# Kernel optimization log

Hardware: AMD Instinct MI355X
Metric: run time of the kernel (lower is better)

Reference implementation:

```python
import jax, jax.numpy as jnp
import numpy as np

N = 50000      # num nodes
E = 800000     # num edges
IN = 128       # in_channels
OUT = 128      # out_channels
H = 8          # num_heads
HD = OUT // H  # out_channels_conv (per-head dim)
EDIM = 16      # edge_dim
HID = 512      # hidden_dim of dst MLP


def layer_norm(x, w, b, eps=1e-5):
    m = jnp.mean(x, axis=-1, keepdims=True)
    v = jnp.var(x, axis=-1, keepdims=True)
    return (x - m) * jax.lax.rsqrt(v + eps) * w + b


def setup_inputs() -> dict:
    key = jax.random.key(0)
    ks = jax.random.split(key, 16)
    lin = lambda k, i, o: jax.random.normal(k, (i, o), jnp.float32) / np.sqrt(i)
    return {
        "x": jax.random.normal(ks[0], (N, IN), jnp.float32),
        "edge_attr": jax.random.normal(ks[1], (E, EDIM), jnp.float32),
        "edge_index": jax.random.randint(ks[2], (2, E), 0, N),
        "Wq": lin(ks[3], IN, OUT), "bq": jnp.zeros((OUT,), jnp.float32),
        "Wk": lin(ks[4], IN, OUT), "bk": jnp.zeros((OUT,), jnp.float32),
        "Wv": lin(ks[5], IN, OUT), "bv": jnp.zeros((OUT,), jnp.float32),
        "Ws": lin(ks[6], IN, OUT), "bs": jnp.zeros((OUT,), jnp.float32),
        "We": lin(ks[7], EDIM, OUT), "be": jnp.zeros((OUT,), jnp.float32),
        "Wp": lin(ks[8], OUT, OUT), "bp": jnp.zeros((OUT,), jnp.float32),
        "ln_a_w": jnp.ones((IN,), jnp.float32), "ln_a_b": jnp.zeros((IN,), jnp.float32),
        "ln_m_w": jnp.ones((OUT,), jnp.float32), "ln_m_b": jnp.zeros((OUT,), jnp.float32),
        "W1": lin(ks[9], OUT, HID), "b1": jnp.zeros((HID,), jnp.float32),
        "W2": lin(ks[10], HID, OUT), "b2": jnp.zeros((OUT,), jnp.float32),
    }


def reference(x, edge_attr, edge_index, Wq, bq, Wk, bk, Wv, bv, Ws, bs, We, be,
              Wp, bp, ln_a_w, ln_a_b, ln_m_w, ln_m_b, W1, b1, W2, b2):
    src, dst = edge_index[0], edge_index[1]

    x_skip = x
    xn = layer_norm(x, ln_a_w, ln_a_b)           # pre-attention LN
    x_r = xn @ Ws + bs                           # lin_self

    q = (xn @ Wq + bq).reshape(N, H, HD)
    k = (xn @ Wk + bk).reshape(N, H, HD)
    v = (xn @ Wv + bv).reshape(N, H, HD)
    e = (edge_attr @ We + be).reshape(E, H, HD)

    # edge-indexed attention: score(edge) = <q[dst], k[src]+e> / sqrt(HD)
    kj = k[src] + e                                              # [E,H,HD]
    scores = jnp.einsum('ehd,ehd->eh', q[dst], kj) / np.sqrt(HD)  # [E,H]

    # segment softmax over incoming edges of each dst node
    smax = jax.ops.segment_max(scores, dst, num_segments=N)     # [N,H]
    smax = jnp.where(jnp.isfinite(smax), smax, 0.0)             # guard empty segments
    ex = jnp.exp(scores - smax[dst])                            # [E,H]
    denom = jax.ops.segment_sum(ex, dst, num_segments=N)        # [N,H]
    alpha = ex / jnp.maximum(denom[dst], 1e-16)                 # [E,H]

    msg = (v[src] + e) * alpha[..., None]                       # [E,H,HD]
    out = jax.ops.segment_sum(msg, dst, num_segments=N).reshape(N, OUT)

    out = (out + x_r) @ Wp + bp                                 # projection
    out = out + x_skip                                          # residual

    # dst-node MLP with pre-LN and residual
    h = layer_norm(out, ln_m_w, ln_m_b)
    nodes_new = jax.nn.gelu(h @ W1 + b1) @ W2 + b2 + out
    return nodes_new, edge_attr
```

## Files before the change

kernel.cpp:

```cpp
#include <hip/hip_runtime.h>
#include <math.h>

#define N_NODES 50000
#define N_EDGES 800000

typedef __attribute__((ext_vector_type(8))) short bf16x8;
typedef __attribute__((ext_vector_type(4))) float f32x4;

__device__ __forceinline__ short f2bf(float f){
  unsigned u = __float_as_uint(f);
  unsigned r = (u + 0x7FFFu + ((u >> 16) & 1u)) >> 16;
  return (short)r;
}

__device__ __forceinline__ float gelu_f(float x){
  float z = 0.7978845608028654f*(x + 0.044715f*x*x*x);
  float e = __expf(2.0f*z);
  return 0.5f*x*(2.0f - 2.0f/(e + 1.0f));
}

__global__ __launch_bounds__(256) void k_tconv(const float* __restrict__ W, short* __restrict__ Wt,
                                               int K, int Nn){
  int i = blockIdx.x*256 + threadIdx.x;
  if (i < K*Nn){
    int n = i / K, k = i - n*K;
    Wt[(size_t)n*K + k] = f2bf(W[(size_t)k*Nn + n]);
  }
}

struct TC6 { const float* src[6]; short* dst[6]; };
__global__ __launch_bounds__(256) void k_tconv6(TC6 t){
  int b = blockIdx.y;
  const float* W = t.src[b];
  short* Wt = t.dst[b];
  int i = blockIdx.x*256 + threadIdx.x;
  int n = i >> 7, k = i & 127;
  Wt[n*128 + k] = f2bf(W[k*128 + n]);
}

__global__ __launch_bounds__(256) void k_wqm(const float* __restrict__ Wq, const float* __restrict__ We,
                                             const float* __restrict__ bq,
                                             float* __restrict__ Wqm, float* __restrict__ bqm){
  int i = blockIdx.x*256 + threadIdx.x;
  if (i < 16384){
    int k = i >> 7, j = i & 127;
    int h = j >> 4, c = j & 15;
    float s = 0.f;
    #pragma unroll
    for (int dd = 0; dd < 16; ++dd)
      s += Wq[k*128 + h*16 + dd] * We[c*128 + h*16 + dd];
    Wqm[i] = s;
    if (k == 0){
      float t = 0.f;
      #pragma unroll
      for (int dd = 0; dd < 16; ++dd)
        t += bq[h*16 + dd] * We[c*128 + h*16 + dd];
      bqm[j] = t;
    }
  }
}

__global__ __launch_bounds__(256) void k_deg(const int* __restrict__ dst, int* __restrict__ deg){
  int i = blockIdx.x*256 + threadIdx.x;
  if (i < N_EDGES) atomicAdd(&deg[dst[i]], 1);
}

__global__ __launch_bounds__(256) void k_bsum(const int* __restrict__ deg,
                                              int* __restrict__ bsum, int* __restrict__ hist){
  __shared__ int lhist[64];
  __shared__ int wred[4];
  int tid = threadIdx.x;
  int i = blockIdx.x*256 + tid;
  if (tid < 64) lhist[tid] = 0;
  __syncthreads();
  int v = (i < N_NODES) ? deg[i] : 0;
  if (i < N_NODES) atomicAdd(&lhist[v > 63 ? 63 : v], 1);
  int s = v;
  #pragma unroll
  for (int sh = 32; sh >= 1; sh >>= 1) s += __shfl_xor(s, sh, 64);
  if ((tid & 63) == 0) wred[tid >> 6] = s;
  __syncthreads();
  if (tid == 0) bsum[blockIdx.x] = wred[0] + wred[1] + wred[2] + wred[3];
  if (tid < 64){ int c = lhist[tid]; if (c) atomicAdd(&hist[tid], c); }
}

__global__ __launch_bounds__(256) void k_bscan(const int* __restrict__ bsum, int* __restrict__ bbase,
                                               const int* __restrict__ hist, int* __restrict__ histcur){
  __shared__ int wsum[4];
  int tid = threadIdx.x;
  int v = (tid < 196) ? bsum[tid] : 0;
  int incl = v;
  #pragma unroll
  for (int s = 1; s < 64; s <<= 1){
    int t = __shfl_up(incl, s, 64);
    if ((tid & 63) >= s) incl += t;
  }
  if ((tid & 63) == 63) wsum[tid >> 6] = incl;
  __syncthreads();
  if (tid == 0){ int c = 0; for (int j = 0; j < 4; ++j){ int t = wsum[j]; wsum[j] = c; c += t; } }
  __syncthreads();
  if (tid < 196) bbase[tid] = wsum[tid >> 6] + (incl - v);
  if (tid < 64){
    int h = hist[tid];
    int inc = h;
    #pragma unroll
    for (int s = 1; s < 64; s <<= 1){
      int t = __shfl_up(inc, s, 64);
      if (tid >= s) inc += t;
    }
    int total = __shfl(inc, 63, 64);
    histcur[tid] = total - inc;
  }
}

__global__ __launch_bounds__(256) void k_apply(const int* __restrict__ deg, const int* __restrict__ bbase,
                                               int* __restrict__ off, int* __restrict__ cursor){
  __shared__ int wsum[4];
  int tid = threadIdx.x;
  int i = blockIdx.x*256 + tid;
  int v = (i < N_NODES) ? deg[i] : 0;
  int incl = v;
  #pragma unroll
  for (int s = 1; s < 64; s <<= 1){
    int t = __shfl_up(incl, s, 64);
    if ((tid & 63) >= s) incl += t;
  }
  if ((tid & 63) == 63) wsum[tid >> 6] = incl;
  __syncthreads();
  if (tid == 0){ int c = 0; for (int j = 0; j < 4; ++j){ int t = wsum[j]; wsum[j] = c; c += t; } }
  __syncthreads();
  int excl = bbase[blockIdx.x] + wsum[tid >> 6] + (incl - v);
  if (i < N_NODES){
    off[i] = excl; cursor[i] = excl;
    if (i == N_NODES-1) off[N_NODES] = excl + v;
  }
}

__global__ __launch_bounds__(256) void k_scatter(const int* __restrict__ dst, const int* __restrict__ src,
                                                 int* __restrict__ cursor, int2* __restrict__ ebuf){
  int i = blockIdx.x*256 + threadIdx.x;
  if (i < N_EDGES){
    int d = dst[i];
    int pos = atomicAdd(&cursor[d], 1);
    ebuf[pos] = make_int2(src[i], i);
  }
}

__global__ __launch_bounds__(256) void k_perm(const int* __restrict__ deg, const int* __restrict__ off,
                                              int* __restrict__ histcur,
                                              int* __restrict__ perm, int2* __restrict__ rng){
  __shared__ int lhist[64];
  __shared__ int lbase[64];
  int tid = threadIdx.x;
  int i = blockIdx.x*256 + tid;
  if (tid < 64) lhist[tid] = 0;
  __syncthreads();
  int d = 0, b = 0, loc = 0;
  bool ok = i < N_NODES;
  if (ok){
    d = deg[i];
    b = d > 63 ? 63 : d;
    loc = atomicAdd(&lhist[b], 1);
  }
  __syncthreads();
  if (tid < 64){
    int c = lhist[tid];
    lbase[tid] = c ? atomicAdd(&histcur[tid], c) : 0;
  }
  __syncthreads();
  if (ok){
    int pos = lbase[b] + loc;
    perm[pos] = i;
    int o = off[i];
    rng[pos] = make_int2(o, o + d);
  }
}

__global__ __launch_bounds__(256) void k_nodeproj(
  const float* __restrict__ x, const float* __restrict__ lnw, const float* __restrict__ lnb,
  const short* __restrict__ Wtq, const short* __restrict__ Wtqm,
  const short* __restrict__ Wtk, const short* __restrict__ Wtv, const short* __restrict__ Wts,
  const float* __restrict__ bq, const float* __restrict__ bqm,
  const float* __restrict__ bk, const float* __restrict__ bv, const float* __restrict__ bs,
  ushort* __restrict__ qb, ushort* __restrict__ qweb,
  ushort* __restrict__ kb, ushort* __restrict__ vb, float* __restrict__ xr)
{
  __shared__ short A[64][136];
  int tid = threadIdx.x;
  int rbase = blockIdx.x * 64;

  {
    int r = tid >> 2, j = tid & 3;
    int row = rbase + r;
    bool ok = row < N_NODES;
    const float* xp = x + (size_t)row*128 + j*32;
    float vals[32];
    #pragma unroll
    for (int i = 0; i < 8; ++i){
      float4 t = ok ? *(const float4*)(xp + i*4) : make_float4(0,0,0,0);
      vals[i*4+0]=t.x; vals[i*4+1]=t.y; vals[i*4+2]=t.z; vals[i*4+3]=t.w;
    }
    float s = 0.f, s2 = 0.f;
    #pragma unroll
    for (int i = 0; i < 32; ++i){ s += vals[i]; s2 += vals[i]*vals[i]; }
    s  += __shfl_xor(s, 1, 64);  s  += __shfl_xor(s, 2, 64);
    s2 += __shfl_xor(s2, 1, 64); s2 += __shfl_xor(s2, 2, 64);
    float mean = s * 0.0078125f;
    float var  = s2 * 0.0078125f - mean*mean;
    float rstd = rsqrtf(var + 1e-5f);
    #pragma unroll
    for (int i = 0; i < 32; ++i){
      int col = j*32 + i;
      float xn = (vals[i]-mean)*rstd*lnw[col] + lnb[col];
      A[r][col] = f2bf(xn);
    }
  }
  __syncthreads();

  int lane = tid & 63, wave = tid >> 6;
  int row16 = lane & 15, kg = lane >> 4;
  int cb = wave * 32;

  auto gemm = [&](const short* __restrict__ B, const float* __restrict__ bias,
                  float* __restrict__ Of, ushort* __restrict__ Ob){
    f32x4 acc[4][2] = {};
    #pragma unroll
    for (int kk = 0; kk < 128; kk += 32){
      int k0 = kk + kg*8;
      bf16x8 a0 = *(const bf16x8*)&A[ 0 + row16][k0];
      bf16x8 a1 = *(const bf16x8*)&A[16 + row16][k0];
      bf16x8 a2 = *(const bf16x8*)&A[32 + row16][k0];
      bf16x8 a3 = *(const bf16x8*)&A[48 + row16][k0];
      bf16x8 b0 = *(const bf16x8*)&B[(size_t)(cb +      row16)*128 + k0];
      bf16x8 b1 = *(const bf16x8*)&B[(size_t)(cb + 16 + row16)*128 + k0];
      acc[0][0] = __builtin_amdgcn_mfma_f32_16x16x32_bf16(a0, b0, acc[0][0], 0,0,0);
      acc[1][0] = __builtin_amdgcn_mfma_f32_16x16x32_bf16(a1, b0, acc[1][0], 0,0,0);
      acc[2][0] = __builtin_amdgcn_mfma_f32_16x16x32_bf16(a2, b0, acc[2][0], 0,0,0);
      acc[3][0] = __builtin_amdgcn_mfma_f32_16x16x32_bf16(a3, b0, acc[3][0], 0,0,0);
      acc[0][1] = __builtin_amdgcn_mfma_f32_16x16x32_bf16(a0, b1, acc[0][1], 0,0,0);
      acc[1][1] = __builtin_amdgcn_mfma_f32_16x16x32_bf16(a1, b1, acc[1][1], 0,0,0);
      acc[2][1] = __builtin_amdgcn_mfma_f32_16x16x32_bf16(a2, b1, acc[2][1], 0,0,0);
      acc[3][1] = __builtin_amdgcn_mfma_f32_16x16x32_bf16(a3, b1, acc[3][1], 0,0,0);
    }
    float bv0 = bias[cb + row16], bv1 = bias[cb + 16 + row16];
    #pragma unroll
    for (int rt = 0; rt < 4; ++rt){
      #pragma unroll
      for (int i = 0; i < 4; ++i){
        int row = rbase + rt*16 + kg*4 + i;
        if (row < N_NODES){
          float v0 = acc[rt][0][i] + bv0;
          float v1 = acc[rt][1][i] + bv1;
          if (Of){
            Of[(size_t)row*128 + cb      + row16] = v0;
            Of[(size_t)row*128 + cb + 16 + row16] = v1;
          } else {
            Ob[(size_t)row*128 + cb      + row16] = (ushort)f2bf(v0);
            Ob[(size_t)row*128 + cb + 16 + row16] = (ushort)f2bf(v1);
          }
        }
      }
    }
  };
  gemm(Wtq,  bq,  nullptr, qb);
  gemm(Wtqm, bqm, nullptr, qweb);
  gemm(Wtk,  bk,  nullptr, kb);
  gemm(Wtv,  bv,  nullptr, vb);
  gemm(Wts,  bs,  xr,  nullptr);
}

__global__ __launch_bounds__(256) void k_agg(
  const ushort* __restrict__ qb, const ushort* __restrict__ qweb,
  const ushort* __restrict__ kbf, const ushort* __restrict__ vbf,
  const float* __restrict__ edge_attr, const float* __restrict__ We, const float* __restrict__ be,
  const int2* __restrict__ ebuf, const int* __restrict__ perm, const int2* __restrict__ rng,
  float* __restrict__ xr)
{
  int tid = threadIdx.x;
  int gid = blockIdx.x*8 + (tid >> 5);
  int node = perm[gid];
  int2 r = rng[gid];
  int beg = r.x, end = r.y;
  int l = tid & 31;
  int d0 = l*4;
  int h  = l >> 2;
  int c0 = (l & 3)*4;

  uint2 qw = *(const uint2*)&qb[(size_t)node*128 + d0];
  float4 qv = make_float4(__uint_as_float(qw.x<<16), __uint_as_float(qw.x&0xffff0000u),
                          __uint_as_float(qw.y<<16), __uint_as_float(qw.y&0xffff0000u));
  uint2 qew = *(const uint2*)&qweb[(size_t)node*128 + h*16 + c0];
  float4 qe = make_float4(__uint_as_float(qew.x<<16), __uint_as_float(qew.x&0xffff0000u),
                          __uint_as_float(qew.y<<16), __uint_as_float(qew.y&0xffff0000u));
  float m = -INFINITY, den = 0.f;
  float4 va = make_float4(0,0,0,0);
  float4 S  = make_float4(0,0,0,0);

  int p = beg;
  for (; p + 4 <= end; p += 4){
    int2 pr0 = ebuf[p+0];
    int2 pr1 = ebuf[p+1];
    int2 pr2 = ebuf[p+2];
    int2 pr3 = ebuf[p+3];
    uint2 kw0 = *(const uint2*)&kbf[(size_t)pr0.x*128 + d0];
    uint2 kw1 = *(const uint2*)&kbf[(size_t)pr1.x*128 + d0];
    uint2 kw2 = *(const uint2*)&kbf[(size_t)pr2.x*128 + d0];
    uint2 kw3 = *(const uint2*)&kbf[(size_t)pr3.x*128 + d0];
    uint2 vw0 = *(const uint2*)&vbf[(size_t)pr0.x*128 + d0];
    uint2 vw1 = *(const uint2*)&vbf[(size_t)pr1.x*128 + d0];
    uint2 vw2 = *(const uint2*)&vbf[(size_t)pr2.x*128 + d0];
    uint2 vw3 = *(const uint2*)&vbf[(size_t)pr3.x*128 + d0];
    float4 e0 = *(const float4*)&edge_attr[(size_t)pr0.y*16 + c0];
    float4 e1 = *(const float4*)&edge_attr[(size_t)pr1.y*16 + c0];
    float4 e2 = *(const float4*)&edge_attr[(size_t)pr2.y*16 + c0];
    float4 e3 = *(const float4*)&edge_attr[(size_t)pr3.y*16 + c0];

    float p0 = qv.x*__uint_as_float(kw0.x<<16) + qv.y*__uint_as_float(kw0.x&0xffff0000u)
             + qv.z*__uint_as_float(kw0.y<<16) + qv.w*__uint_as_float(kw0.y&0xffff0000u)
             + qe.x*e0.x + qe.y*e0.y + qe.z*e0.z + qe.w*e0.w;
    float p1 = qv.x*__uint_as_float(kw1.x<<16) + qv.y*__uint_as_float(kw1.x&0xffff0000u)
             + qv.z*__uint_as_float(kw1.y<<16) + qv.w*__uint_as_float(kw1.y&0xffff0000u)
             + qe.x*e1.x + qe.y*e1.y + qe.z*e1.z + qe.w*e1.w;
    float p2 = qv.x*__uint_as_float(kw2.x<<16) + qv.y*__uint_as_float(kw2.x&0xffff0000u)
             + qv.z*__uint_as_float(kw2.y<<16) + qv.w*__uint_as_float(kw2.y&0xffff0000u)
             + qe.x*e2.x + qe.y*e2.y + qe.z*e2.z + qe.w*e2.w;
    float p3 = qv.x*__uint_as_float(kw3.x<<16) + qv.y*__uint_as_float(kw3.x&0xffff0000u)
             + qv.z*__uint_as_float(kw3.y<<16) + qv.w*__uint_as_float(kw3.y&0xffff0000u)
             + qe.x*e3.x + qe.y*e3.y + qe.z*e3.z + qe.w*e3.w;
    p0 += __shfl_xor(p0,1,64); p0 += __shfl_xor(p0,2,64);
    p1 += __shfl_xor(p1,1,64); p1 += __shfl_xor(p1,2,64);
    p2 += __shfl_xor(p2,1,64); p2 += __shfl_xor(p2,2,64);
    p3 += __shfl_xor(p3,1,64); p3 += __shfl_xor(p3,2,64);
    float sc0 = p0*0.25f, sc1 = p1*0.25f, sc2 = p2*0.25f, sc3 = p3*0.25f;
    float mn = fmaxf(fmaxf(m, fmaxf(sc0,sc1)), fmaxf(sc2,sc3));
    float corr = __expf(m - mn);
    float w0 = __expf(sc0 - mn), w1 = __expf(sc1 - mn);
    float w2 = __expf(sc2 - mn), w3 = __expf(sc3 - mn);
    den = den*corr + ((w0+w1)+(w2+w3));
    va.x = va.x*corr + (w0*__uint_as_float(vw0.x<<16)        + w1*__uint_as_float(vw1.x<<16))
                     + (w2*__uint_as_float(vw2.x<<16)        + w3*__uint_as_float(vw3.x<<16));
    va.y = va.y*corr + (w0*__uint_as_float(vw0.x&0xffff0000u)+ w1*__uint_as_float(vw1.x&0xffff0000u))
                     + (w2*__uint_as_float(vw2.x&0xffff0000u)+ w3*__uint_as_float(vw3.x&0xffff0000u));
    va.z = va.z*corr + (w0*__uint_as_float(vw0.y<<16)        + w1*__uint_as_float(vw1.y<<16))
                     + (w2*__uint_as_float(vw2.y<<16)        + w3*__uint_as_float(vw3.y<<16));
    va.w = va.w*corr + (w0*__uint_as_float(vw0.y&0xffff0000u)+ w1*__uint_as_float(vw1.y&0xffff0000u))
                     + (w2*__uint_as_float(vw2.y&0xffff0000u)+ w3*__uint_as_float(vw3.y&0xffff0000u));
    S.x = S.x*corr + (w0*e0.x + w1*e1.x) + (w2*e2.x + w3*e3.x);
    S.y = S.y*corr + (w0*e0.y + w1*e1.y) + (w2*e2.y + w3*e3.y);
    S.z = S.z*corr + (w0*e0.z + w1*e1.z) + (w2*e2.z + w3*e3.z);
    S.w = S.w*corr + (w0*e0.w + w1*e1.w) + (w2*e2.w + w3*e3.w);
    m = mn;
  }
  for (; p < end; ++p){
    int2 pr = ebuf[p];
    uint2 kw = *(const uint2*)&kbf[(size_t)pr.x*128 + d0];
    uint2 vw = *(const uint2*)&vbf[(size_t)pr.x*128 + d0];
    float4 ev = *(const float4*)&edge_attr[(size_t)pr.y*16 + c0];
    float pp = qv.x*__uint_as_float(kw.x<<16) + qv.y*__uint_as_float(kw.x&0xffff0000u)
             + qv.z*__uint_as_float(kw.y<<16) + qv.w*__uint_as_float(kw.y&0xffff0000u)
             + qe.x*ev.x + qe.y*ev.y + qe.z*ev.z + qe.w*ev.w;
    pp += __shfl_xor(pp,1,64); pp += __shfl_xor(pp,2,64);
    float sc = pp*0.25f;
    float mn = fmaxf(m, sc);
    float corr = __expf(m - mn);
    float pe = __expf(sc - mn);
    den = den*corr + pe;
    va.x = va.x*corr + pe*__uint_as_float(vw.x<<16);
    va.y = va.y*corr + pe*__uint_as_float(vw.x&0xffff0000u);
    va.z = va.z*corr + pe*__uint_as_float(vw.y<<16);
    va.w = va.w*corr + pe*__uint_as_float(vw.y&0xffff0000u);
    S.x = S.x*corr + pe*ev.x;
    S.y = S.y*corr + pe*ev.y;
    S.z = S.z*corr + pe*ev.z;
    S.w = S.w*corr + pe*ev.w;
    m = mn;
  }

  if (end > beg){
    float inv = 1.0f/den;
    float4 acc = va;
    int gb = (tid & 63) & 60;
    #pragma unroll
    for (int g = 0; g < 4; ++g){
      float s0 = __shfl(S.x, gb+g, 64);
      float s1 = __shfl(S.y, gb+g, 64);
      float s2 = __shfl(S.z, gb+g, 64);
      float s3 = __shfl(S.w, gb+g, 64);
      float4 w0 = *(const float4*)&We[(g*4+0)*128 + d0];
      float4 w1 = *(const float4*)&We[(g*4+1)*128 + d0];
      float4 w2 = *(const float4*)&We[(g*4+2)*128 + d0];
      float4 w3 = *(const float4*)&We[(g*4+3)*128 + d0];
      acc.x += s0*w0.x + s1*w1.x + s2*w2.x + s3*w3.x;
      acc.y += s0*w0.y + s1*w1.y + s2*w2.y + s3*w3.y;
      acc.z += s0*w0.z + s1*w1.z + s2*w2.z + s3*w3.z;
      acc.w += s0*w0.w + s1*w1.w + s2*w2.w + s3*w3.w;
    }
    float4 bev = *(const float4*)&be[d0];
    float4 xv = *(const float4*)&xr[(size_t)node*128 + d0];
    xv.x += acc.x*inv + bev.x;
    xv.y += acc.y*inv + bev.y;
    xv.z += acc.z*inv + bev.z;
    xv.w += acc.w*inv + bev.w;
    *(float4*)&xr[(size_t)node*128 + d0] = xv;
  }
}

__global__ __launch_bounds__(256) void k_post(
  const float* __restrict__ aggout, const float* __restrict__ x,
  const short* __restrict__ Wtp, const float* __restrict__ bp,
  const float* __restrict__ lnw, const float* __restrict__ lnb,
  float* __restrict__ res, short* __restrict__ A2)
{
  __shared__ short A[64][136];
  __shared__ float rf[64][132];
  int tid = threadIdx.x;
  int rbase = blockIdx.x * 64;

  {
    int r = tid >> 2, j = tid & 3;
    int row = rbase + r;
    const float* p = aggout + (size_t)row*128 + j*32;
    #pragma unroll
    for (int i = 0; i < 8; ++i){
      float4 t = *(const float4*)(p + i*4);
      int c = j*32 + i*4;
      A[r][c+0] = f2bf(t.x); A[r][c+1] = f2bf(t.y);
      A[r][c+2] = f2bf(t.z); A[r][c+3] = f2bf(t.w);
    }
  }
  __syncthreads();

  int lane = tid & 63, wave = tid >> 6;
  int row16 = lane & 15, kg = lane >> 4;
  int cb = wave * 32;

  f32x4 acc[4][2] = {};
  #pragma unroll
  for (int kk = 0; kk < 128; kk += 32){
    int k0 = kk + kg*8;
    bf16x8 a0 = *(const bf16x8*)&A[ 0 + row16][k0];
    bf16x8 a1 = *(const bf16x8*)&A[16 + row16][k0];
    bf16x8 a2 = *(const bf16x8*)&A[32 + row16][k0];
    bf16x8 a3 = *(const bf16x8*)&A[48 + row16][k0];
    bf16x8 b0 = *(const bf16x8*)&Wtp[(size_t)(cb +      row16)*128 + k0];
    bf16x8 b1 = *(const bf16x8*)&Wtp[(size_t)(cb + 16 + row16)*128 + k0];
    acc[0][0] = __builtin_amdgcn_mfma_f32_16x16x32_bf16(a0, b0, acc[0][0], 0,0,0);
    acc[1][0] = __builtin_amdgcn_mfma_f32_16x16x32_bf16(a1, b0, acc[1][0], 0,0,0);
    acc[2][0] = __builtin_amdgcn_mfma_f32_16x16x32_bf16(a2, b0, acc[2][0], 0,0,0);
    acc[3][0] = __builtin_amdgcn_mfma_f32_16x16x32_bf16(a3, b0, acc[3][0], 0,0,0);
    acc[0][1] = __builtin_amdgcn_mfma_f32_16x16x32_bf16(a0, b1, acc[0][1], 0,0,0);
    acc[1][1] = __builtin_amdgcn_mfma_f32_16x16x32_bf16(a1, b1, acc[1][1], 0,0,0);
    acc[2][1] = __builtin_amdgcn_mfma_f32_16x16x32_bf16(a2, b1, acc[2][1], 0,0,0);
    acc[3][1] = __builtin_amdgcn_mfma_f32_16x16x32_bf16(a3, b1, acc[3][1], 0,0,0);
  }
  float bv0 = bp[cb + row16], bv1 = bp[cb + 16 + row16];
  #pragma unroll
  for (int rt = 0; rt < 4; ++rt){
    #pragma unroll
    for (int i = 0; i < 4; ++i){
      int rl = rt*16 + kg*4 + i;
      int row = rbase + rl;
      float v0 = acc[rt][0][i] + bv0;
      float v1 = acc[rt][1][i] + bv1;
      if (row < N_NODES){
        v0 += x[(size_t)row*128 + cb      + row16];
        v1 += x[(size_t)row*128 + cb + 16 + row16];
        res[(size_t)row*128 + cb      + row16] = v0;
        res[(size_t)row*128 + cb + 16 + row16] = v1;
      }
      rf[rl][cb      + row16] = v0;
      rf[rl][cb + 16 + row16] = v1;
    }
  }
  __syncthreads();

  {
    int r = tid >> 2, j = tid & 3;
    int row = rbase + r;
    float vals[32];
    #pragma unroll
    for (int i = 0; i < 8; ++i){
      float4 t = *(const float4*)&rf[r][j*32 + i*4];
      vals[i*4+0]=t.x; vals[i*4+1]=t.y; vals[i*4+2]=t.z; vals[i*4+3]=t.w;
    }
    float s = 0.f, s2 = 0.f;
    #pragma unroll
    for (int i = 0; i < 32; ++i){ s += vals[i]; s2 += vals[i]*vals[i]; }
    s  += __shfl_xor(s, 1, 64);  s  += __shfl_xor(s, 2, 64);
    s2 += __shfl_xor(s2, 1, 64); s2 += __shfl_xor(s2, 2, 64);
    float mean = s * 0.0078125f;
    float var  = s2 * 0.0078125f - mean*mean;
    float rstd = rsqrtf(var + 1e-5f);
    #pragma unroll
    for (int i = 0; i < 32; ++i){
      int col = j*32 + i;
      float xn = (vals[i]-mean)*rstd*lnw[col] + lnb[col];
      A2[(size_t)row*128 + col] = f2bf(xn);
    }
  }
}

__global__ __launch_bounds__(256) void k_mlp1(
  const short* __restrict__ A2, const short* __restrict__ W1t, const float* __restrict__ b1,
  short* __restrict__ hid)
{
  __shared__ short A[64][136];
  int tid = threadIdx.x;
  int rbase = blockIdx.x * 64;
  int ch = blockIdx.y;
  for (int idx = tid; idx < 1024; idx += 256){
    int r = idx >> 4, g = idx & 15;
    *(uint4*)&A[r][g*8] = *(const uint4*)&A2[((size_t)(rbase + r))*128 + g*8];
  }
  __syncthreads();

  int lane = tid & 63, wave = tid >> 6;
  int row16 = lane & 15, kg = lane >> 4;
  int cb = ch*256 + wave*64;

  f32x4 acc[4][4] = {};
  #pragma unroll
  for (int kk = 0; kk < 128; kk += 32){
    int k0 = kk + kg*8;
    bf16x8 a[4], b[4];
    #pragma unroll
    for (int rt = 0; rt < 4; ++rt) a[rt] = *(const bf16x8*)&A[rt*16 + row16][k0];
    #pragma unroll
    for (int ct = 0; ct < 4; ++ct) b[ct] = *(const bf16x8*)&W1t[(size_t)(cb + ct*16 + row16)*128 + k0];
    #pragma unroll
    for (int rt = 0; rt < 4; ++rt)
      #pragma unroll
      for (int ct = 0; ct < 4; ++ct)
        acc[rt][ct] = __builtin_amdgcn_mfma_f32_16x16x32_bf16(a[rt], b[ct], acc[rt][ct], 0,0,0);
  }
  float bv[4];
  #pragma unroll
  for (int ct = 0; ct < 4; ++ct) bv[ct] = b1[cb + ct*16 + row16];
  #pragma unroll
  for (int rt = 0; rt < 4; ++rt){
    #pragma unroll
    for (int ct = 0; ct < 4; ++ct){
      #pragma unroll
      for (int i = 0; i < 4; ++i){
        int row = rbase + rt*16 + kg*4 + i;
        hid[(size_t)row*512 + cb + ct*16 + row16] = f2bf(gelu_f(acc[rt][ct][i] + bv[ct]));
      }
    }
  }
}

__global__ __launch_bounds__(256) void k_mlp2(
  const short* __restrict__ hid, const short* __restrict__ W2t, const float* __restrict__ b2,
  const float* __restrict__ res, float* __restrict__ out)
{
  __shared__ short A[64][136];
  int tid = threadIdx.x;
  int rbase = blockIdx.x * 64;
  int lane = tid & 63, wave = tid >> 6;
  int row16 = lane & 15, kg = lane >> 4;
  int cb = wave * 32;

  f32x4 acc[4][2] = {};
  for (int kc = 0; kc < 4; ++kc){
    __syncthreads();
    for (int idx = tid; idx < 1024; idx += 256){
      int r = idx >> 4, g = idx & 15;
      *(uint4*)&A[r][g*8] = *(const uint4*)&hid[((size_t)(rbase + r))*512 + kc*128 + g*8];
    }
    __syncthreads();
    #pragma unroll
    for (int kk = 0; kk < 128; kk += 32){
      int k0 = kk + kg*8;
      bf16x8 a0 = *(const bf16x8*)&A[ 0 + row16][k0];
      bf16x8 a1 = *(const bf16x8*)&A[16 + row16][k0];
      bf16x8 a2 = *(const bf16x8*)&A[32 + row16][k0];
      bf16x8 a3 = *(const bf16x8*)&A[48 + row16][k0];
      bf16x8 b0 = *(const bf16x8*)&W2t[(size_t)(cb +      row16)*512 + kc*128 + k0];
      bf16x8 b1 = *(const bf16x8*)&W2t[(size_t)(cb + 16 + row16)*512 + kc*128 + k0];
      acc[0][0] = __builtin_amdgcn_mfma_f32_16x16x32_bf16(a0, b0, acc[0][0], 0,0,0);
      acc[1][0] = __builtin_amdgcn_mfma_f32_16x16x32_bf16(a1, b0, acc[1][0], 0,0,0);
      acc[2][0] = __builtin_amdgcn_mfma_f32_16x16x32_bf16(a2, b0, acc[2][0], 0,0,0);
      acc[3][0] = __builtin_amdgcn_mfma_f32_16x16x32_bf16(a3, b0, acc[3][0], 0,0,0);
      acc[0][1] = __builtin_amdgcn_mfma_f32_16x16x32_bf16(a0, b1, acc[0][1], 0,0,0);
      acc[1][1] = __builtin_amdgcn_mfma_f32_16x16x32_bf16(a1, b1, acc[1][1], 0,0,0);
      acc[2][1] = __builtin_amdgcn_mfma_f32_16x16x32_bf16(a2, b1, acc[2][1], 0,0,0);
      acc[3][1] = __builtin_amdgcn_mfma_f32_16x16x32_bf16(a3, b1, acc[3][1], 0,0,0);
    }
  }
  float bv0 = b2[cb + row16], bv1 = b2[cb + 16 + row16];
  #pragma unroll
  for (int rt = 0; rt < 4; ++rt){
    #pragma unroll
    for (int i = 0; i < 4; ++i){
      int row = rbase + rt*16 + kg*4 + i;
      if (row < N_NODES){
        out[(size_t)row*128 + cb      + row16] = acc[rt][0][i] + bv0 + res[(size_t)row*128 + cb      + row16];
        out[(size_t)row*128 + cb + 16 + row16] = acc[rt][1][i] + bv1 + res[(size_t)row*128 + cb + 16 + row16];
      }
    }
  }
}

extern "C" void kernel_launch(void* const* d_in, const int* in_sizes, int n_in,
                              void* d_out, int out_size, void* d_ws, size_t ws_size,
                              hipStream_t stream)
{
  const float* x        = (const float*)d_in[0];
  const float* edge_attr= (const float*)d_in[1];
  const int*   edge_index=(const int*)d_in[2];
  const float* Wq = (const float*)d_in[3];  const float* bq = (const float*)d_in[4];
  const float* Wk = (const float*)d_in[5];  const float* bk = (const float*)d_in[6];
  const float* Wv = (const float*)d_in[7];  const float* bv = (const float*)d_in[8];
  const float* Wss= (const float*)d_in[9];  const float* bss= (const float*)d_in[10];
  const float* We = (const float*)d_in[11]; const float* be = (const float*)d_in[12];
  const float* Wp = (const float*)d_in[13]; const float* bp = (const float*)d_in[14];
  const float* lnaw=(const float*)d_in[15]; const float* lnab=(const float*)d_in[16];
  const float* lnmw=(const float*)d_in[17]; const float* lnmb=(const float*)d_in[18];
  const float* W1 = (const float*)d_in[19]; const float* b1 = (const float*)d_in[20];
  const float* W2 = (const float*)d_in[21]; const float* b2 = (const float*)d_in[22];

  float* ws = (float*)d_ws;
  const size_t NP128 = 6406144;
  const size_t NPH   = 3203072;
  ushort* qb   = (ushort*)ws;
  ushort* qweb = (ushort*)(ws + NPH);
  ushort* kbf  = (ushort*)(ws + 2*NPH);
  ushort* vbf  = (ushort*)(ws + 3*NPH);
  float*  xr   = ws + 4*NPH;
  float*  res  = ws + 4*NPH + NP128;
  short* wts   = (short*)(ws + 25624576);
  short* Wtq   = wts;
  short* Wtk   = wts + 16384;
  short* Wtv   = wts + 32768;
  short* Wts_  = wts + 49152;
  short* Wtp   = wts + 65536;
  short* Wtqm  = wts + 81920;
  short* W1t   = wts + 98304;
  short* W2t   = wts + 163840;
  float* Wqm_f = ws + 25624576 + 114688;
  float* bqm   = Wqm_f + 16384;
  int*   iw    = (int*)(bqm + 128);
  int* deg     = iw;
  int* hist    = iw + 50000;
  int* histcur = iw + 50064;
  int* bsum    = iw + 50128;
  int* bbase   = iw + 50324;
  int* off     = iw + 50520;
  int* cursor  = iw + 100521;
  int* perm    = iw + 150521;
  int2* rng    = (int2*)(iw + 200522);
  int2* ebuf   = (int2*)(iw + 300522);

  short* A2   = (short*)qb;
  short* hid  = (short*)qweb;

  const int* srcIdx = edge_index;
  const int* dstIdx = edge_index + N_EDGES;

  k_wqm<<<64, 256, 0, stream>>>(Wq, We, bq, Wqm_f, bqm);
  TC6 tc;
  tc.src[0]=Wq; tc.src[1]=Wk; tc.src[2]=Wv; tc.src[3]=Wss; tc.src[4]=Wp; tc.src[5]=Wqm_f;
  tc.dst[0]=Wtq; tc.dst[1]=Wtk; tc.dst[2]=Wtv; tc.dst[3]=Wts_; tc.dst[4]=Wtp; tc.dst[5]=Wtqm;
  k_tconv6<<<dim3(64,6), 256, 0, stream>>>(tc);
  k_tconv<<<256, 256, 0, stream>>>(W1, W1t, 128, 512);
  k_tconv<<<256, 256, 0, stream>>>(W2, W2t, 512, 128);

  hipMemsetAsync(deg, 0, 50064*sizeof(int), stream);
  k_deg<<<(N_EDGES+255)/256, 256, 0, stream>>>(dstIdx, deg);
  k_bsum<<<196, 256, 0, stream>>>(deg, bsum, hist);
  k_bscan<<<1, 256, 0, stream>>>(bsum, bbase, hist, histcur);
  k_apply<<<196, 256, 0, stream>>>(deg, bbase, off, cursor);
  k_scatter<<<(N_EDGES+255)/256, 256, 0, stream>>>(dstIdx, srcIdx, cursor, ebuf);
  k_perm<<<(N_NODES+255)/256, 256, 0, stream>>>(deg, off, histcur, perm, rng);

  k_nodeproj<<<782, 256, 0, stream>>>(x, lnaw, lnab, Wtq, Wtqm, Wtk, Wtv, Wts_,
                                      bq, bqm, bk, bv, bss, qb, qweb, kbf, vbf, xr);
  k_agg<<<N_NODES/8, 256, 0, stream>>>(qb, qweb, kbf, vbf, edge_attr, We, be,
                                       ebuf, perm, rng, xr);
  k_post<<<782, 256, 0, stream>>>(xr, x, Wtp, bp, lnmw, lnmb, res, A2);
  k_mlp1<<<dim3(782,2), 256, 0, stream>>>(A2, W1t, b1, hid);
  k_mlp2<<<782, 256, 0, stream>>>(hid, W2t, b2, res, (float*)d_out);

  hipMemcpyAsync((float*)d_out + (size_t)N_NODES*128, edge_attr,
                 (size_t)N_EDGES*16*sizeof(float), hipMemcpyDeviceToDevice, stream);
}
```

Before: 369.9 us.

## Pre-sort edge attributes to bf16 in CSR order and unroll aggregation by eight

The scatter kernel now writes each edge's attributes, converted to bf16 and placed in dst-sorted order, into a scratch buffer that aliases the residual workspace. The aggregation kernel then reads these contiguously instead of gathering fp32 rows by original edge id, and reads only the source index from a smaller int array. The aggregation main loop is also unrolled to 8 edges, with a 4-edge step after it. This aims to cut gather traffic and random access in the aggregation kernel, at the cost of extra write traffic in scatter and some loss of precision from rounding edge features to bf16.

```diff
diff --git a/kernel.cpp b/kernel.cpp
--- a/kernel.cpp
+++ b/kernel.cpp
@@ -12,12 +12,18 @@
   unsigned r = (u + 0x7FFFu + ((u >> 16) & 1u)) >> 16;
   return (short)r;
 }
+__device__ __forceinline__ unsigned pkbf(float lo, float hi){
+  return (unsigned)(unsigned short)f2bf(lo) | ((unsigned)(unsigned short)f2bf(hi) << 16);
+}
 
 __device__ __forceinline__ float gelu_f(float x){
   float z = 0.7978845608028654f*(x + 0.044715f*x*x*x);
   float e = __expf(2.0f*z);
   return 0.5f*x*(2.0f - 2.0f/(e + 1.0f));
 }
+
+#define BF_LO(u) __uint_as_float((u)<<16)
+#define BF_HI(u) __uint_as_float((u)&0xffff0000u)
 
 __global__ __launch_bounds__(256) void k_tconv(const float* __restrict__ W, short* __restrict__ Wt,
                                                int K, int Nn){
@@ -137,12 +143,22 @@
 }
 
 __global__ __launch_bounds__(256) void k_scatter(const int* __restrict__ dst, const int* __restrict__ src,
-                                                 int* __restrict__ cursor, int2* __restrict__ ebuf){
+                                                 const float* __restrict__ edge_attr,
+                                                 int* __restrict__ cursor,
+                                                 int* __restrict__ esrc, ushort* __restrict__ eab){
   int i = blockIdx.x*256 + threadIdx.x;
   if (i < N_EDGES){
     int d = dst[i];
     int pos = atomicAdd(&cursor[d], 1);
-    ebuf[pos] = make_int2(src[i], i);
+    esrc[pos] = src[i];
+    const float* ea = edge_attr + (size_t)i*16;
+    float4 a = *(const float4*)(ea+0), b = *(const float4*)(ea+4),
+           c = *(const float4*)(ea+8), e = *(const float4*)(ea+12);
+    uint4 o0, o1;
+    o0.x = pkbf(a.x,a.y); o0.y = pkbf(a.z,a.w); o0.z = pkbf(b.x,b.y); o0.w = pkbf(b.z,b.w);
+    o1.x = pkbf(c.x,c.y); o1.y = pkbf(c.z,c.w); o1.z = pkbf(e.x,e.y); o1.w = pkbf(e.z,e.w);
+    *(uint4*)&eab[(size_t)pos*16]     = o0;
+    *(uint4*)&eab[(size_t)pos*16 + 8] = o1;
   }
 }
 
@@ -272,8 +288,8 @@
 __global__ __launch_bounds__(256) void k_agg(
   const ushort* __restrict__ qb, const ushort* __restrict__ qweb,
   const ushort* __restrict__ kbf, const ushort* __restrict__ vbf,
-  const float* __restrict__ edge_attr, const float* __restrict__ We, const float* __restrict__ be,
-  const int2* __restrict__ ebuf, const int* __restrict__ perm, const int2* __restrict__ rng,
+  const ushort* __restrict__ eab, const float* __restrict__ We, const float* __restrict__ be,
+  const int* __restrict__ esrc, const int* __restrict__ perm, const int2* __restrict__ rng,
   float* __restrict__ xr)
 {
   int tid = threadIdx.x;
@@ -287,92 +303,85 @@
   int c0 = (l & 3)*4;
 
   uint2 qw = *(const uint2*)&qb[(size_t)node*128 + d0];
-  float4 qv = make_float4(__uint_as_float(qw.x<<16), __uint_as_float(qw.x&0xffff0000u),
-                          __uint_as_float(qw.y<<16), __uint_as_float(qw.y&0xffff0000u));
+  float4 qv = make_float4(BF_LO(qw.x), BF_HI(qw.x), BF_LO(qw.y), BF_HI(qw.y));
   uint2 qew = *(const uint2*)&qweb[(size_t)node*128 + h*16 + c0];
-  float4 qe = make_float4(__uint_as_float(qew.x<<16), __uint_as_float(qew.x&0xffff0000u),
-                          __uint_as_float(qew.y<<16), __uint_as_float(qew.y&0xffff0000u));
+  float4 qe = make_float4(BF_LO(qew.x), BF_HI(qew.x), BF_LO(qew.y), BF_HI(qew.y));
   float m = -INFINITY, den = 0.f;
   float4 va = make_float4(0,0,0,0);
   float4 S  = make_float4(0,0,0,0);
 
   int p = beg;
-  for (; p + 4 <= end; p += 4){
-    int2 pr0 = ebuf[p+0];
-    int2 pr1 = ebuf[p+1];
-    int2 pr2 = ebuf[p+2];
-    int2 pr3 = ebuf[p+3];
-    uint2 kw0 = *(const uint2*)&kbf[(size_t)pr0.x*128 + d0];
-    uint2 kw1 = *(const uint2*)&kbf[(size_t)pr1.x*128 + d0];
-    uint2 kw2 = *(const uint2*)&kbf[(size_t)pr2.x*128 + d0];
-    uint2 kw3 = *(const uint2*)&kbf[(size_t)pr3.x*128 + d0];
-    uint2 vw0 = *(const uint2*)&vbf[(size_t)pr0.x*128 + d0];
-    uint2 vw1 = *(const uint2*)&vbf[(size_t)pr1.x*128 + d0];
-    uint2 vw2 = *(const uint2*)&vbf[(size_t)pr2.x*128 + d0];
-    uint2 vw3 = *(const uint2*)&vbf[(size_t)pr3.x*128 + d0];
-    float4 e0 = *(const float4*)&edge_attr[(size_t)pr0.y*16 + c0];
-    float4 e1 = *(const float4*)&edge_attr[(size_t)pr1.y*16 + c0];
-    float4 e2 = *(const float4*)&edge_attr[(size_t)pr2.y*16 + c0];
-    float4 e3 = *(const float4*)&edge_attr[(size_t)pr3.y*16 + c0];
-
-    float p0 = qv.x*__uint_as_float(kw0.x<<16) + qv.y*__uint_as_float(kw0.x&0xffff0000u)
-             + qv.z*__uint_as_float(kw0.y<<16) + qv.w*__uint_as_float(kw0.y&0xffff0000u)
-             + qe.x*e0.x + qe.y*e0.y + qe.z*e0.z + qe.w*e0.w;
-    float p1 = qv.x*__uint_as_float(kw1.x<<16) + qv.y*__uint_as_float(kw1.x&0xffff0000u)
-             + qv.z*__uint_as_float(kw1.y<<16) + qv.w*__uint_as_float(kw1.y&0xffff0000u)
-             + qe.x*e1.x + qe.y*e1.y + qe.z*e1.z + qe.w*e1.w;
-    float p2 = qv.x*__uint_as_float(kw2.x<<16) + qv.y*__uint_as_float(kw2.x&0xffff0000u)
-             + qv.z*__uint_as_float(kw2.y<<16) + qv.w*__uint_as_float(kw2.y&0xffff0000u)
-             + qe.x*e2.x + qe.y*e2.y + qe.z*e2.z + qe.w*e2.w;
-    float p3 = qv.x*__uint_as_float(kw3.x<<16) + qv.y*__uint_as_float(kw3.x&0xffff0000u)
-             + qv.z*__uint_as_float(kw3.y<<16) + qv.w*__uint_as_float(kw3.y&0xffff0000u)
-             + qe.x*e3.x + qe.y*e3.y + qe.z*e3.z + qe.w*e3.w;
-    p0 += __shfl_xor(p0,1,64); p0 += __shfl_xor(p0,2,64);
-    p1 += __shfl_xor(p1,1,64); p1 += __shfl_xor(p1,2,64);
-    p2 += __shfl_xor(p2,1,64); p2 += __shfl_xor(p2,2,64);
-    p3 += __shfl_xor(p3,1,64); p3 += __shfl_xor(p3,2,64);
-    float sc0 = p0*0.25f, sc1 = p1*0.25f, sc2 = p2*0.25f, sc3 = p3*0.25f;
-    float mn = fmaxf(fmaxf(m, fmaxf(sc0,sc1)), fmaxf(sc2,sc3));
-    float corr = __expf(m - mn);
-    float w0 = __expf(sc0 - mn), w1 = __expf(sc1 - mn);
-    float w2 = __expf(sc2 - mn), w3 = __expf(sc3 - mn);
-    den = den*corr + ((w0+w1)+(w2+w3));
-    va.x = va.x*corr + (w0*__uint_as_float(vw0.x<<16)        + w1*__uint_as_float(vw1.x<<16))
-                     + (w2*__uint_as_float(vw2.x<<16)        + w3*__uint_as_float(vw3.x<<16));
-    va.y = va.y*corr + (w0*__uint_as_float(vw0.x&0xffff0000u)+ w1*__uint_as_float(vw1.x&0xffff0000u))
-                     + (w2*__uint_as_float(vw2.x&0xffff0000u)+ w3*__uint_as_float(vw3.x&0xffff0000u));
-    va.z = va.z*corr + (w0*__uint_as_float(vw0.y<<16)        + w1*__uint_as_float(vw1.y<<16))
-                     + (w2*__uint_as_float(vw2.y<<16)        + w3*__uint_as_float(vw3.y<<16));
-    va.w = va.w*corr + (w0*__uint_as_float(vw0.y&0xffff0000u)+ w1*__uint_as_float(vw1.y&0xffff0000u))
-                     + (w2*__uint_as_float(vw2.y&0xffff0000u)+ w3*__uint_as_float(vw3.y&0xffff0000u));
-    S.x = S.x*corr + (w0*e0.x + w1*e1.x) + (w2*e2.x + w3*e3.x);
-    S.y = S.y*corr + (w0*e0.y + w1*e1.y) + (w2*e2.y + w3*e3.y);
-    S.z = S.z*corr + (w0*e0.z + w1*e1.z) + (w2*e2.z + w3*e3.z);
-    S.w = S.w*corr + (w0*e0.w + w1*e1.w) + (w2*e2.w + w3*e3.w);
-    m = mn;
-  }
+
+#define AGG_STEP(J)                                                            \
+  {                                                                            \
+    int sidx[J];                                                               \
+    _Pragma("unroll")                                                          \
+    for (int j = 0; j < J; ++j) sidx[j] = esrc[p+j];                           \
+    uint2 kw[J], vw[J], ew[J];                                                 \
+    _Pragma("unroll")                                                          \
+    for (int j = 0; j < J; ++j){                                               \
+      kw[j] = *(const uint2*)&kbf[(size_t)sidx[j]*128 + d0];                   \
+      vw[j] = *(const uint2*)&vbf[(size_t)sidx[j]*128 + d0];                   \
+      ew[j] = *(const uint2*)&eab[(size_t)(p+j)*16 + c0];                      \
+    }                                                                          \
+    float sc[J];                                                               \
+    _Pragma("unroll")                                                          \
+    for (int j = 0; j < J; ++j){                                               \
+      float pp = qv.x*BF_LO(kw[j].x) + qv.y*BF_HI(kw[j].x)                     \
+               + qv.z*BF_LO(kw[j].y) + qv.w*BF_HI(kw[j].y)                     \
+               + qe.x*BF_LO(ew[j].x) + qe.y*BF_HI(ew[j].x)                     \
+               + qe.z*BF_LO(ew[j].y) + qe.w*BF_HI(ew[j].y);                    \
+      pp += __shfl_xor(pp,1,64); pp += __shfl_xor(pp,2,64);                    \
+      sc[j] = pp*0.25f;                                                        \
+    }                                                                          \
+    float mn = m;                                                              \
+    _Pragma("unroll")                                                          \
+    for (int j = 0; j < J; ++j) mn = fmaxf(mn, sc[j]);                         \
+    float corr = __expf(m - mn);                                               \
+    float w[J]; float ds = 0.f;                                                \
+    _Pragma("unroll")                                                          \
+    for (int j = 0; j < J; ++j){ w[j] = __expf(sc[j]-mn); ds += w[j]; }        \
+    den = den*corr + ds;                                                       \
+    float ax=0.f, ay=0.f, az=0.f, aw2=0.f, sx=0.f, sy=0.f, sz=0.f, sw=0.f;     \
+    _Pragma("unroll")                                                          \
+    for (int j = 0; j < J; ++j){                                               \
+      ax += w[j]*BF_LO(vw[j].x); ay += w[j]*BF_HI(vw[j].x);                    \
+      az += w[j]*BF_LO(vw[j].y); aw2+= w[j]*BF_HI(vw[j].y);                    \
+      sx += w[j]*BF_LO(ew[j].x); sy += w[j]*BF_HI(ew[j].x);                    \
+      sz += w[j]*BF_LO(ew[j].y); sw += w[j]*BF_HI(ew[j].y);                    \
+    }                                                                          \
+    va.x = va.x*corr + ax; va.y = va.y*corr + ay;                              \
+    va.z = va.z*corr + az; va.w = va.w*corr + aw2;                             \
+    S.x  = S.x *corr + sx; S.y  = S.y *corr + sy;                              \
+    S.z  = S.z *corr + sz; S.w  = S.w *corr + sw;                              \
+    m = mn;                                                                    \
+  }
+
+  for (; p + 8 <= end; p += 8) AGG_STEP(8)
+  for (; p + 4 <= end; p += 4) AGG_STEP(4)
   for (; p < end; ++p){
-    int2 pr = ebuf[p];
-    uint2 kw = *(const uint2*)&kbf[(size_t)pr.x*128 + d0];
-    uint2 vw = *(const uint2*)&vbf[(size_t)pr.x*128 + d0];
-    float4 ev = *(const float4*)&edge_attr[(size_t)pr.y*16 + c0];
-    float pp = qv.x*__uint_as_float(kw.x<<16) + qv.y*__uint_as_float(kw.x&0xffff0000u)
-             + qv.z*__uint_as_float(kw.y<<16) + qv.w*__uint_as_float(kw.y&0xffff0000u)
-             + qe.x*ev.x + qe.y*ev.y + qe.z*ev.z + qe.w*ev.w;
+    int s = esrc[p];
+    uint2 kw = *(const uint2*)&kbf[(size_t)s*128 + d0];
+    uint2 vw = *(const uint2*)&vbf[(size_t)s*128 + d0];
+    uint2 ew = *(const uint2*)&eab[(size_t)p*16 + c0];
+    float pp = qv.x*BF_LO(kw.x) + qv.y*BF_HI(kw.x)
+             + qv.z*BF_LO(kw.y) + qv.w*BF_HI(kw.y)
+             + qe.x*BF_LO(ew.x) + qe.y*BF_HI(ew.x)
+             + qe.z*BF_LO(ew.y) + qe.w*BF_HI(ew.y);
     pp += __shfl_xor(pp,1,64); pp += __shfl_xor(pp,2,64);
     float sc = pp*0.25f;
     float mn = fmaxf(m, sc);
     float corr = __expf(m - mn);
     float pe = __expf(sc - mn);
     den = den*corr + pe;
-    va.x = va.x*corr + pe*__uint_as_float(vw.x<<16);
-    va.y = va.y*corr + pe*__uint_as_float(vw.x&0xffff0000u);
-    va.z = va.z*corr + pe*__uint_as_float(vw.y<<16);
-    va.w = va.w*corr + pe*__uint_as_float(vw.y&0xffff0000u);
-    S.x = S.x*corr + pe*ev.x;
-    S.y = S.y*corr + pe*ev.y;
-    S.z = S.z*corr + pe*ev.z;
-    S.w = S.w*corr + pe*ev.w;
+    va.x = va.x*corr + pe*BF_LO(vw.x);
+    va.y = va.y*corr + pe*BF_HI(vw.x);
+    va.z = va.z*corr + pe*BF_LO(vw.y);
+    va.w = va.w*corr + pe*BF_HI(vw.y);
+    S.x = S.x*corr + pe*BF_LO(ew.x);
+    S.y = S.y*corr + pe*BF_HI(ew.x);
+    S.z = S.z*corr + pe*BF_LO(ew.y);
+    S.w = S.w*corr + pe*BF_HI(ew.y);
     m = mn;
   }
 
@@ -628,6 +637,7 @@
   ushort* vbf  = (ushort*)(ws + 3*NPH);
   float*  xr   = ws + 4*NPH;
   float*  res  = ws + 4*NPH + NP128;
+  ushort* eab  = (ushort*)res;
   short* wts   = (short*)(ws + 25624576);
   short* Wtq   = wts;
   short* Wtk   = wts + 16384;
@@ -649,7 +659,7 @@
   int* cursor  = iw + 100521;
   int* perm    = iw + 150521;
   int2* rng    = (int2*)(iw + 200522);
-  int2* ebuf   = (int2*)(iw + 300522);
+  int* esrc    = iw + 300522;
 
   short* A2   = (short*)qb;
   short* hid  = (short*)qweb;
@@ -670,13 +680,13 @@
   k_bsum<<<196, 256, 0, stream>>>(deg, bsum, hist);
   k_bscan<<<1, 256, 0, stream>>>(bsum, bbase, hist, histcur);
   k_apply<<<196, 256, 0, stream>>>(deg, bbase, off, cursor);
-  k_scatter<<<(N_EDGES+255)/256, 256, 0, stream>>>(dstIdx, srcIdx, cursor, ebuf);
+  k_scatter<<<(N_EDGES+255)/256, 256, 0, stream>>>(dstIdx, srcIdx, edge_attr, cursor, esrc, eab);
   k_perm<<<(N_NODES+255)/256, 256, 0, stream>>>(deg, off, histcur, perm, rng);
 
   k_nodeproj<<<782, 256, 0, stream>>>(x, lnaw, lnab, Wtq, Wtqm, Wtk, Wtv, Wts_,
                                       bq, bqm, bk, bv, bss, qb, qweb, kbf, vbf, xr);
-  k_agg<<<N_NODES/8, 256, 0, stream>>>(qb, qweb, kbf, vbf, edge_attr, We, be,
-                                       ebuf, perm, rng, xr);
+  k_agg<<<N_NODES/8, 256, 0, stream>>>(qb, qweb, kbf, vbf, eab, We, be,
+                                       esrc, perm, rng, xr);
   k_post<<<782, 256, 0, stream>>>(xr, x, Wtp, bp, lnmw, lnmb, res, A2);
   k_mlp1<<<dim3(782,2), 256, 0, stream>>>(A2, W1t, b1, hid);
   k_mlp2<<<782, 256, 0, stream>>>(hid, W2t, b2, res, (float*)d_out);
```

Result: no change. 367.4 us (-0.7%).
